# Performance work log

Hardware: AMD Instinct MI355X
Metric: run time of the kernel (lower is better)

## Reference

```python
import jax, jax.numpy as jnp
import numpy as np

VOCAB, D, HEADS, FF, LAYERS = 30522, 768, 12, 3072, 4
CHUNK, OVERLAP, EXT = 50, 7, 64
SAMPLE_N, TOPK, PAD = 8, 3, 0
MU = jnp.array([1.0, 0.9, 0.7, 0.5, 0.3, 0.1, -0.1, -0.3, -0.5, -0.7, -0.9], jnp.float32)
SIGMA = 0.1


def layernorm(x, g, b, eps=1e-12):
    m = x.mean(-1, keepdims=True)
    v = ((x - m) ** 2).mean(-1, keepdims=True)
    return (x - m) * jax.lax.rsqrt(v + eps) * g + b


def ck_context(x, conv_w, conv_b):
    # ConstantPad1d((0,2)) + Conv1d(k=3) + ReLU + L2-normalize; x: [..., L, D]
    L = x.shape[-2]
    pad = [(0, 0)] * (x.ndim - 2) + [(0, 2), (0, 0)]
    xp = jnp.pad(x, pad)
    y = conv_b + sum(jnp.einsum('...li,io->...lo', xp[..., k:k + L, :], conv_w[k]) for k in range(3))
    y = jax.nn.relu(y)
    return y / jnp.maximum(jnp.linalg.norm(y, axis=-1, keepdims=True), 1e-12)


def bert_layer(x, mask, Wq, bq, Wk, bk, Wv, bv, Wo, bo, g1, be1, W1, bf1, W2, bf2, g2, be2):
    N, L, _ = x.shape
    dh = D // HEADS
    split = lambda h: h.reshape(N, L, HEADS, dh)
    q, k, v = split(x @ Wq + bq), split(x @ Wk + bk), split(x @ Wv + bv)
    s = jnp.einsum('nqhd,nkhd->nhqk', q, k) / jnp.sqrt(jnp.asarray(dh, x.dtype))
    s = jnp.where(mask[:, None, None, :], s, -1e4)
    ctx = jnp.einsum('nhqk,nkhd->nqhd', jax.nn.softmax(s, -1), v).reshape(N, L, D)
    x = layernorm(x + ctx @ Wo + bo, g1, be1)
    h = jax.nn.gelu(x @ W1 + bf1, approximate=False)
    return layernorm(x + h @ W2 + bf2, g2, be2)


def setup_inputs():
    ks = jax.random.split(jax.random.key(0), 24)
    B, Lq, Ldoc = 32, 30, 4000
    f = lambda i, shape, s=0.02: jax.random.normal(ks[i], shape, jnp.float32) * s
    lens = jax.random.randint(ks[20], (B, 1), 2000, Ldoc, jnp.int32)
    doc_ids = jax.random.randint(ks[1], (B, Ldoc), 1, VOCAB, jnp.int32)
    doc_ids = doc_ids * (jnp.arange(Ldoc)[None, :] < lens)  # variable-length docs, 0 = padding
    return {
        'query_ids': jax.random.randint(ks[0], (B, Lq), 1, VOCAB, jnp.int32),
        'query_mask': jnp.ones((B, Lq), jnp.int32),
        'doc_ids': doc_ids,
        'word_emb': f(2, (VOCAB, D)),
        'pos_emb': f(3, (512, D)),
        'emb_ln_g': jnp.ones((D,), jnp.float32), 'emb_ln_b': jnp.zeros((D,), jnp.float32),
        'conv_w': f(4, (3, D, D)), 'conv_b': jnp.zeros((D,), jnp.float32),
        'kernel_alpha': jnp.ones((11,), jnp.float32),
        'binw_w': jax.random.uniform(ks[5], (1, 11), jnp.float32, -0.01, 0.01),
        'binw_b': jnp.zeros((1,), jnp.float32),
        'cls_w': f(6, (1, D)), 'cls_b': jnp.zeros((1,), jnp.float32),
        'topk_w': jnp.ones((1, TOPK), jnp.float32),
        'Wq': f(7, (LAYERS, D, D)), 'bq': jnp.zeros((LAYERS, D), jnp.float32),
        'Wk': f(8, (LAYERS, D, D)), 'bk': jnp.zeros((LAYERS, D), jnp.float32),
        'Wv': f(9, (LAYERS, D, D)), 'bv': jnp.zeros((LAYERS, D), jnp.float32),
        'Wo': f(10, (LAYERS, D, D)), 'bo': jnp.zeros((LAYERS, D), jnp.float32),
        'ln1_g': jnp.ones((LAYERS, D), jnp.float32), 'ln1_b': jnp.zeros((LAYERS, D), jnp.float32),
        'W1': f(11, (LAYERS, D, FF)), 'bf1': jnp.zeros((LAYERS, FF), jnp.float32),
        'W2': f(12, (LAYERS, FF, D)), 'bf2': jnp.zeros((LAYERS, D), jnp.float32),
        'ln2_g': jnp.ones((LAYERS, D), jnp.float32), 'ln2_b': jnp.zeros((LAYERS, D), jnp.float32),
    }


def reference(query_ids, query_mask, doc_ids, word_emb, pos_emb, emb_ln_g, emb_ln_b,
              conv_w, conv_b, kernel_alpha, binw_w, binw_b, cls_w, cls_b, topk_w,
              Wq, bq, Wk, bk, Wv, bv, Wo, bo, ln1_g, ln1_b, W1, bf1, W2, bf2, ln2_g, ln2_b):
    emb = lambda ids: layernorm(word_emb[ids] + pos_emb[:ids.shape[-1]], emb_ln_g, emb_ln_b)
    d_ids = doc_ids[:, 1:]
    B, Ld0 = d_ids.shape
    Lq = query_ids.shape[1]
    pad_r = EXT - (Ld0 % CHUNK - OVERLAP)  # Ld0 > overlap branch
    d_ids = jnp.pad(d_ids, ((0, 0), (OVERLAP, pad_r)))
    P = (d_ids.shape[1] - EXT) // CHUNK + 1
    win = np.arange(P)[:, None] * CHUNK + np.arange(EXT)[None, :]
    chunks = d_ids[:, win]                                   # [B,P,EXT] (unfold)
    valid = (chunks[..., OVERLAP:-OVERLAP] != PAD).any(-1)   # packed_indices, [B,P]
    chunk_mask = chunks != PAD
    # --- CK kernel-pooling sampler (embeddings detached) ---
    q_ctx = ck_context(jax.lax.stop_gradient(emb(query_ids)), conv_w, conv_b)  # [B,Lq,D]
    d_ctx = ck_context(jax.lax.stop_gradient(emb(chunks)), conv_w, conv_b)     # [B,P,EXT,D]
    cos = jnp.einsum('bqd,bped->bpqe', q_ctx, d_ctx)
    kact = jnp.exp(-(cos[..., None] - MU) ** 2 / (2 * SIGMA ** 2)) * chunk_mask[:, :, None, :, None]
    kres = jnp.log(jnp.maximum(kact.sum(3) * kernel_alpha, 1e-4)) * query_mask[:, None, :, None]
    samp = kres.sum(2) @ binw_w[0] + binw_b[0]               # [B,P]
    samp = jnp.where(valid, samp, 0.0)                       # zeros where not packed
    samp = jnp.where(samp == 0.0, -9000.0, samp)
    # --- top-k chunk routing into BERT (eval path, no cache) ---
    top_idx = jnp.argsort(-samp, axis=1)[:, :SAMPLE_N]       # [B,n]
    sel_ids = jnp.take_along_axis(chunks, top_idx[:, :, None], axis=1).reshape(B * SAMPLE_N, EXT)
    sel_valid = jnp.take_along_axis(valid, top_idx, axis=1)
    qi = jnp.broadcast_to(query_ids[:, None, :], (B, SAMPLE_N, Lq)).reshape(B * SAMPLE_N, Lq)
    qm = jnp.broadcast_to(query_mask[:, None, :], (B, SAMPLE_N, Lq)).reshape(B * SAMPLE_N, Lq)
    ids = jnp.concatenate([qi, sel_ids], 1)                  # [B*n, Lq+EXT]
    am = jnp.concatenate([qm != 0, sel_ids != PAD], 1)
    x = emb(ids)
    for i in range(LAYERS):
        x = bert_layer(x, am, Wq[i], bq[i], Wk[i], bk[i], Wv[i], bv[i], Wo[i], bo[i],
                       ln1_g[i], ln1_b[i], W1[i], bf1[i], W2[i], bf2[i], ln2_g[i], ln2_b[i])
    bscore = (x[:, 0] @ cls_w[0] + cls_b[0]).reshape(B, SAMPLE_N)
    bscore = jax.lax.stop_gradient(bscore)  # torch.set_grad_enabled(False) around BERT path
    bscore = jnp.where(sel_valid, bscore, 0.0)
    scores = jnp.zeros((B, P), bscore.dtype).at[jnp.arange(B)[:, None], top_idx].set(bscore)
    scores = jnp.where(scores == 0.0, -9000.0, scores)
    ssorted = -jnp.sort(-scores, axis=1)
    ssorted = jnp.where(ssorted <= -8900.0, 0.0, ssorted)
    return (ssorted[:, :TOPK] * topk_w[0]).sum(1)            # [B]
```

## Files before the change

### kernel.cpp

```cpp
#include <hip/hip_runtime.h>
#include <hip/hip_bf16.h>
#include <cstring>
#include <cmath>

#define NBAT 32
#define LQ 30
#define NP 80
#define NSEGC 2560
#define DD 768
#define KC 6912
#define LB 94
#define FF 3072

typedef unsigned short u16;
typedef __attribute__((__ext_vector_type__(4))) float f32x4;
typedef __attribute__((__ext_vector_type__(8))) short s16x8;
typedef __attribute__((__ext_vector_type__(8))) _Float16 f16x8;

__constant__ float MU_C[11] = {1.0f,0.9f,0.7f,0.5f,0.3f,0.1f,-0.1f,-0.3f,-0.5f,-0.7f,-0.9f};

__device__ __forceinline__ float wsum(float v) {
#pragma unroll
  for (int o = 32; o; o >>= 1) v += __shfl_xor(v, o);
  return v;
}
__device__ __forceinline__ u16 f2b(float f) {
  __hip_bfloat16 h = __float2bfloat16(f);
  u16 u; __builtin_memcpy(&u, &h, 2); return u;
}
__device__ __forceinline__ u16 h_bits(_Float16 h) { u16 u; __builtin_memcpy(&u, &h, 2); return u; }

__device__ __forceinline__ void gll16(const void* g, void* l) {
  __builtin_amdgcn_global_load_lds((const __attribute__((address_space(1))) unsigned*)g,
                                   (__attribute__((address_space(3))) unsigned*)l, 16, 0, 0);
}

template<int AMODE, int DT, int EPI>
__global__ __launch_bounds__(512) void gemm_mid(const u16* __restrict__ A, const u16* __restrict__ BT,
                                                void* __restrict__ Cv, const float* __restrict__ bias,
                                                int M, int N, int K)
{
  __shared__ __align__(16) u16 As[2][128*64];
  __shared__ __align__(16) u16 Bs[2][192*64];
  const int tid = threadIdx.x;
  const int lane = tid & 63;
  const int w = tid >> 6;

  const int NBY = N / 192;
  const int nb = gridDim.x;
  const int q8 = nb >> 3, r8 = nb & 7;
  const int xcd = blockIdx.x & 7, slot = blockIdx.x >> 3;
  const int base8 = (xcd < r8) ? xcd*(q8+1) : r8*(q8+1) + (xcd - r8)*q8;
  const int wk = base8 + slot;
  const long m0 = (long)(wk / NBY) * 128;
  const long n0 = (long)(wk % NBY) * 192;

  const int wr = (w >> 2) * 64;
  const int wc = (w & 3) * 48;

  const int lrow = lane >> 3;
  const int scg  = (lane & 7) ^ lrow;

  long aoff[2], boff[3];
#pragma unroll
  for (int it = 0; it < 2; ++it) {
    const long ga = m0 + it*64 + w*8 + lrow;
    if (AMODE == 0) aoff[it] = ga * (long)K;
    else            aoff[it] = ((ga >> 6) * 66 + (ga & 63)) * 2304L;
  }
#pragma unroll
  for (int it = 0; it < 3; ++it)
    boff[it] = (long)(n0 + it*64 + w*8 + lrow) * (long)K;

  f32x4 acc[4][3] = {};

  const int T = K >> 6;
#pragma unroll
  for (int it = 0; it < 2; ++it)
    gll16(A + aoff[it] + scg*8, &As[0][(it*64 + w*8) * 64]);
#pragma unroll
  for (int it = 0; it < 3; ++it)
    gll16(BT + boff[it] + scg*8, &Bs[0][(it*64 + w*8) * 64]);

  for (int t = 0; t < T; ++t) {
    const int cb = t & 1;
    if (t + 1 < T) {
      const int k1 = (t + 1) << 6;
#pragma unroll
      for (int it = 0; it < 2; ++it)
        gll16(A + aoff[it] + k1 + scg*8, &As[cb ^ 1][(it*64 + w*8) * 64]);
#pragma unroll
      for (int it = 0; it < 3; ++it)
        gll16(BT + boff[it] + k1 + scg*8, &Bs[cb ^ 1][(it*64 + w*8) * 64]);
      asm volatile("s_waitcnt vmcnt(5)" ::: "memory");
    } else {
      asm volatile("s_waitcnt vmcnt(0)" ::: "memory");
    }
    __builtin_amdgcn_s_barrier();
    __builtin_amdgcn_sched_barrier(0);
#pragma unroll
    for (int kk = 0; kk < 2; ++kk) {
      const int cc = kk*4 + (lane >> 4);
      const int sw = (cc ^ (lane & 7)) * 8;
      if constexpr (DT == 0) {
        s16x8 af[4], bg[3];
#pragma unroll
        for (int m = 0; m < 4; ++m)
          af[m] = *(const s16x8*)&As[cb][(wr + m*16 + (lane & 15))*64 + sw];
#pragma unroll
        for (int n = 0; n < 3; ++n)
          bg[n] = *(const s16x8*)&Bs[cb][(wc + n*16 + (lane & 15))*64 + sw];
#pragma unroll
        for (int m = 0; m < 4; ++m)
#pragma unroll
          for (int n = 0; n < 3; ++n)
            acc[m][n] = __builtin_amdgcn_mfma_f32_16x16x32_bf16(af[m], bg[n], acc[m][n], 0, 0, 0);
      } else {
        f16x8 af[4], bg[3];
#pragma unroll
        for (int m = 0; m < 4; ++m)
          af[m] = *(const f16x8*)&As[cb][(wr + m*16 + (lane & 15))*64 + sw];
#pragma unroll
        for (int n = 0; n < 3; ++n)
          bg[n] = *(const f16x8*)&Bs[cb][(wc + n*16 + (lane & 15))*64 + sw];
#pragma unroll
        for (int m = 0; m < 4; ++m)
#pragma unroll
          for (int n = 0; n < 3; ++n)
            acc[m][n] = __builtin_amdgcn_mfma_f32_16x16x32_f16(af[m], bg[n], acc[m][n], 0, 0, 0);
      }
    }
    __builtin_amdgcn_sched_barrier(0);
    __builtin_amdgcn_s_barrier();
  }
#pragma unroll
  for (int m = 0; m < 4; ++m) {
    const long r0 = m0 + wr + m*16 + (lane >> 4)*4;
#pragma unroll
    for (int n = 0; n < 3; ++n) {
      const long c = n0 + wc + n*16 + (lane & 15);
#pragma unroll
      for (int j = 0; j < 4; ++j) {
        const float val = acc[m][n][j];
        if constexpr (EPI == 0) {
          ((float*)Cv)[(r0 + j) * (long)N + c] = val;
        } else if constexpr (EPI == 1) {
          const float tg = val + bias[c];
          ((u16*)Cv)[(r0 + j) * (long)N + c] = f2b(0.5f * tg * (1.0f + erff(tg * 0.70710678118654752440f)));
        } else if constexpr (EPI == 2) {
          ((u16*)Cv)[(r0 + j) * (long)N + c] = f2b(val);
        } else {
          ((u16*)Cv)[(r0 + j) * (long)N + c] = f2b(val + bias[c]);
        }
      }
    }
  }
  (void)M;
}

__global__ __launch_bounds__(256) void k_transpose_tile(const float* __restrict__ src, u16* __restrict__ dst,
                                                        int K, int N)
{
  __shared__ float tile[64][65];
  const int kb = blockIdx.x * 64, nb = blockIdx.y * 64;
  const int tx = threadIdx.x & 63, ty = threadIdx.x >> 6;
#pragma unroll
  for (int r = ty; r < 64; r += 4)
    tile[r][tx] = src[(long)(kb + r) * N + nb + tx];
  __syncthreads();
#pragma unroll
  for (int r = ty; r < 64; r += 4)
    dst[(long)(nb + r) * K + kb + tx] = f2b(tile[tx][r]);
}

__global__ __launch_bounds__(256) void k_pack_w3t_tile(const float* __restrict__ conv_w, u16* __restrict__ w3t)
{
  __shared__ float tile[64][65];
  const int t = blockIdx.z;
  const int db = blockIdx.x * 64, ob = blockIdx.y * 64;
  const int tx = threadIdx.x & 63, ty = threadIdx.x >> 6;
#pragma unroll
  for (int r = ty; r < 64; r += 4)
    tile[r][tx] = conv_w[((long)t * 768 + db + r) * 768 + ob + tx];
  __syncthreads();
#pragma unroll
  for (int r = ty; r < 64; r += 4) {
    const float wv = tile[tx][r];
    const _Float16 hi = (_Float16)wv;
    const u16 uh = h_bits(hi);
    const u16 ul = h_bits((_Float16)(wv - (float)hi));
    u16* p = &w3t[(long)(ob + r) * KC + t * 2304 + (db + tx) * 3];
    p[0] = uh; p[1] = uh; p[2] = ul;
  }
}

__global__ void k_pack_qkvbias(const float* __restrict__ bq, const float* __restrict__ bk,
                               const float* __restrict__ bv, float* __restrict__ dst)
{
  const int idx = blockIdx.x*256 + threadIdx.x;
  if (idx >= 4*2304) return;
  const int L = idx / 2304, c = idx % 2304;
  const float* src = (c < 768) ? bq : (c < 1536 ? bk : bv);
  dst[idx] = src[L*768 + (c % 768)];
}

__global__ void k_build_chunks(const int* __restrict__ doc_ids, int* __restrict__ chunks, int* __restrict__ valid)
{
  const int bp = blockIdx.x;
  const int b = bp / NP, p = bp % NP;
  const int e = threadIdx.x;
  const int j = p*50 + e;
  int id = 0;
  const int di = j - 6;
  if (j >= 7 && di < 4000) id = doc_ids[b*4000 + di];
  chunks[bp*64 + e] = id;
  const unsigned long long bal = __ballot(e >= 7 && e < 57 && id != 0);
  if (e == 0) valid[bp] = (bal != 0ULL) ? 1 : 0;
}

__global__ __launch_bounds__(256) void k_emb_conv(const int* __restrict__ chunks,
    const int* __restrict__ query_ids, const float* __restrict__ word_emb,
    const float* __restrict__ pos_emb, const float* __restrict__ g,
    const float* __restrict__ bb, u16* __restrict__ A3, int seg0, int nT)
{
  const int Tl = blockIdx.x*4 + (threadIdx.x >> 6);
  if (Tl >= nT) return;
  const int lane = threadIdx.x & 63;
  const int seg = seg0 + Tl / 66, tok = Tl % 66;
  int id = -1;
  if (seg < NSEGC) { if (tok < 64) id = chunks[seg*64 + tok]; }
  else             { if (tok < LQ) id = query_ids[(seg - NSEGC)*LQ + tok]; }
  const long ob = (long)Tl * 2304;
  if (id < 0) {
#pragma unroll
    for (int j = 0; j < 12; ++j) {
      const int d = lane + 64*j;
      A3[ob + d*3 + 0] = 0; A3[ob + d*3 + 1] = 0; A3[ob + d*3 + 2] = 0;
    }
    return;
  }
  float v[12]; float s = 0.f;
#pragma unroll
  for (int j = 0; j < 12; ++j) {
    const int d = lane + 64*j;
    v[j] = word_emb[(long)id*DD + d] + pos_emb[(long)tok*DD + d];
    s += v[j];
  }
  s = wsum(s);
  const float mean = s * (1.f/768.f);
  float q = 0.f;
#pragma unroll
  for (int j = 0; j < 12; ++j) { const float t = v[j] - mean; q += t*t; }
  q = wsum(q);
  const float rstd = 1.f / sqrtf(q * (1.f/768.f) + 1e-12f);
#pragma unroll
  for (int j = 0; j < 12; ++j) {
    const int d = lane + 64*j;
    const float y = (v[j] - mean) * rstd * g[d] + bb[d];
    const _Float16 hi = (_Float16)y;
    const _Float16 lo = (_Float16)(y - (float)hi);
    const u16 uh = h_bits(hi);
    A3[ob + d*3 + 0] = uh;
    A3[ob + d*3 + 1] = h_bits(lo);
    A3[ob + d*3 + 2] = uh;
  }
}

__global__ __launch_bounds__(256) void k_conv_epi(float* __restrict__ Y, const float* __restrict__ cb)
{
  const int r = blockIdx.x*4 + (threadIdx.x >> 6);
  const int lane = threadIdx.x & 63;
  const long base = (long)r * DD;
  float v[12]; float ss = 0.f;
#pragma unroll
  for (int j = 0; j < 12; ++j) {
    const int d = lane + 64*j;
    float t = Y[base + d] + cb[d];
    t = fmaxf(t, 0.f);
    v[j] = t; ss += t*t;
  }
  ss = wsum(ss);
  const float sc = 1.f / fmaxf(sqrtf(ss), 1e-12f);
#pragma unroll
  for (int j = 0; j < 12; ++j) Y[base + lane + 64*j] = v[j]*sc;
}

__global__ __launch_bounds__(256) void k_cos_pool(const float* __restrict__ Ys,
    const float* __restrict__ qctx, const int* __restrict__ chunks, const int* __restrict__ valid,
    const int* __restrict__ query_mask, const float* __restrict__ alpha,
    const float* __restrict__ binw_w, const float* __restrict__ binw_b,
    float* __restrict__ samp, int seg0)
{
  __shared__ float Qs[15*768];
  __shared__ float cosm[30*64];
  __shared__ float maskf[64];
  __shared__ float qmw[32];
  __shared__ float red[4];
  const int bp = seg0 + blockIdx.x;
  const int b = bp / NP;
  const int tid = threadIdx.x, lane = tid & 63, w = tid >> 6;
  if (tid < 64) maskf[tid] = (chunks[bp*64 + tid] != 0) ? 1.f : 0.f;
  if (tid < LQ) qmw[tid] = (float)query_mask[b*LQ + tid];
  const long dbase = (long)blockIdx.x * 64 * DD;
  const long qrow0 = (long)b * 64;
  for (int pass = 0; pass < 2; ++pass) {
    const int q0 = pass * 15;
    for (int idx = tid; idx < 15*768; idx += 256)
      Qs[idx] = qctx[(qrow0 + q0 + idx/768)*DD + (idx % 768)];
    __syncthreads();
    for (int e = w; e < 64; e += 4) {
      float acc[15];
#pragma unroll
      for (int q = 0; q < 15; ++q) acc[q] = 0.f;
#pragma unroll
      for (int j = 0; j < 12; ++j) {
        const float dv = Ys[dbase + (long)e*DD + lane + 64*j];
#pragma unroll
        for (int q = 0; q < 15; ++q)
          acc[q] += dv * Qs[q*768 + lane + 64*j];
      }
#pragma unroll
      for (int q = 0; q < 15; ++q) {
        const float sv = wsum(acc[q]);
        if (lane == q) cosm[(q0 + q)*64 + e] = sv;
      }
    }
    __syncthreads();
  }
  float part = 0.f;
  for (int pr = tid; pr < 330; pr += 256) {
    const int q = pr / 11, mi = pr % 11;
    const float mu = MU_C[mi];
    float ks = 0.f;
    for (int e = 0; e < 64; ++e) {
      const float c = cosm[q*64 + e] - mu;
      ks += expf(-c*c*50.f) * maskf[e];
    }
    part += logf(fmaxf(ks * alpha[mi], 1e-4f)) * qmw[q] * binw_w[mi];
  }
  part = wsum(part);
  if (lane == 0) red[w] = part;
  __syncthreads();
  if (tid == 0) {
    const float s = red[0] + red[1] + red[2] + red[3] + binw_b[0];
    samp[bp] = (valid[bp] != 0 && s != 0.f) ? s : -9000.0f;
  }
}

__global__ void k_top8(const float* __restrict__ samp, const int* __restrict__ valid,
                       int* __restrict__ topidx, int* __restrict__ selv)
{
  const int b = blockIdx.x;
  const int l = threadIdx.x;
  float v1 = samp[b*NP + l];
  float v2 = (l < NP - 64) ? samp[b*NP + 64 + l] : -3e38f;
  for (int r = 0; r < 8; ++r) {
    float cv; int ci;
    if (v2 > v1) { cv = v2; ci = l + 64; } else { cv = v1; ci = l; }
#pragma unroll
    for (int o = 32; o; o >>= 1) {
      const float ov = __shfl_xor(cv, o);
      const int   oi = __shfl_xor(ci, o);
      if (ov > cv || (ov == cv && oi < ci)) { cv = ov; ci = oi; }
    }
    if (l == 0) { topidx[b*8 + r] = ci; selv[b*8 + r] = valid[b*NP + ci]; }
    if (ci == l)      v1 = -3e38f;
    if (ci == l + 64) v2 = -3e38f;
  }
}

__global__ __launch_bounds__(256) void k_bert_emb(const int* __restrict__ chunks,
    const int* __restrict__ query_ids, const int* __restrict__ query_mask,
    const int* __restrict__ topidx, const float* __restrict__ word_emb,
    const float* __restrict__ pos_emb, const float* __restrict__ g, const float* __restrict__ bb,
    float* __restrict__ xf, u16* __restrict__ xb, int* __restrict__ am, int n0)
{
  const int Tl = blockIdx.x*4 + (threadIdx.x >> 6);
  const int lane = threadIdx.x & 63;
  const int nl = Tl / LB, l = Tl % LB;
  const int n = n0 + nl;
  const int b = n >> 3, jj = n & 7;
  int id, amv;
  if (l < LQ) { id = query_ids[b*LQ + l]; amv = (query_mask[b*LQ + l] != 0) ? 1 : 0; }
  else { const int p = topidx[b*8 + jj]; id = chunks[(b*NP + p)*64 + (l - LQ)]; amv = (id != 0) ? 1 : 0; }
  if (lane == 0) am[n*LB + l] = amv;
  const long ob = (long)Tl * DD;
  float v[12]; float s = 0.f;
#pragma unroll
  for (int j = 0; j < 12; ++j) {
    const int d = lane + 64*j;
    v[j] = word_emb[(long)id*DD + d] + pos_emb[(long)l*DD + d];
    s += v[j];
  }
  s = wsum(s);
  const float mean = s * (1.f/768.f);
  float q = 0.f;
#pragma unroll
  for (int j = 0; j < 12; ++j) { const float t = v[j] - mean; q += t*t; }
  q = wsum(q);
  const float rstd = 1.f / sqrtf(q*(1.f/768.f) + 1e-12f);
#pragma unroll
  for (int j = 0; j < 12; ++j) {
    const int d = lane + 64*j;
    const float y = (v[j] - mean)*rstd*g[d] + bb[d];
    xf[ob + d] = y;
    xb[ob + d] = f2b(y);
  }
}

__global__ __launch_bounds__(384) void k_attn_mfma(const u16* __restrict__ qkvb,
    const int* __restrict__ am, u16* __restrict__ ctxb, int n0)
{
  __shared__ __align__(16) u16 Kb[96*72];
  __shared__ __align__(16) u16 Vt[64*104];
  __shared__ __align__(16) u16 Pl[6*16*104];
  __shared__ float maskb[96];
  const int nb = blockIdx.x;
  const int nl = nb / 12, h = nb % 12;
  const int tid = threadIdx.x, lane = tid & 63, w = tid >> 6;
  const int hoff = h * 64;
  const long rowbase = (long)nl * LB;

  for (int idx = tid; idx < 96*8; idx += 384) {
    const int l = idx >> 3, seg = idx & 7;
    s16x8 z = {};
    if (l < LB) z = *(const s16x8*)&qkvb[(rowbase + l)*2304 + 768 + hoff + seg*8];
    *(s16x8*)&Kb[l*72 + seg*8] = z;
  }
  for (int idx = tid; idx < 96*64; idx += 384) {
    const int j = idx >> 6, d = idx & 63;
    Vt[d*104 + j] = (j < LB) ? qkvb[(rowbase + j)*2304 + 1536 + hoff + d] : (u16)0;
  }
  if (tid < 96) maskb[tid] = (tid < LB && am[(n0 + nl)*LB + tid] != 0) ? 1.f : 0.f;
  __syncthreads();

  const int rt = w;
  s16x8 qf0, qf1;
  {
    int r = rt*16 + (lane & 15); if (r > LB-1) r = LB-1;
    const long qbase = (rowbase + r)*2304 + hoff + (lane >> 4)*8;
    qf0 = *(const s16x8*)&qkvb[qbase];
    qf1 = *(const s16x8*)&qkvb[qbase + 32];
  }
  f32x4 sa[6];
#pragma unroll
  for (int ct = 0; ct < 6; ++ct) {
    sa[ct] = f32x4{0.f,0.f,0.f,0.f};
    const int krow = ct*16 + (lane & 15);
    const s16x8 kf0 = *(const s16x8*)&Kb[krow*72 + (lane >> 4)*8];
    const s16x8 kf1 = *(const s16x8*)&Kb[krow*72 + 32 + (lane >> 4)*8];
    sa[ct] = __builtin_amdgcn_mfma_f32_16x16x32_bf16(qf0, kf0, sa[ct], 0, 0, 0);
    sa[ct] = __builtin_amdgcn_mfma_f32_16x16x32_bf16(qf1, kf1, sa[ct], 0, 0, 0);
  }
  float sv[6][4];
#pragma unroll
  for (int ct = 0; ct < 6; ++ct) {
    const int col = ct*16 + (lane & 15);
    const float mk = maskb[col];
#pragma unroll
    for (int j = 0; j < 4; ++j)
      sv[ct][j] = (mk != 0.f) ? sa[ct][j]*0.125f : -1.0e30f;
  }
  float mx[4], sm[4];
#pragma unroll
  for (int j = 0; j < 4; ++j) {
    float v = sv[0][j];
#pragma unroll
    for (int ct = 1; ct < 6; ++ct) v = fmaxf(v, sv[ct][j]);
#pragma unroll
    for (int o = 1; o < 16; o <<= 1) v = fmaxf(v, __shfl_xor(v, o));
    mx[j] = v;
  }
#pragma unroll
  for (int j = 0; j < 4; ++j) {
    float s = 0.f;
#pragma unroll
    for (int ct = 0; ct < 6; ++ct) { const float p = expf(sv[ct][j] - mx[j]); sv[ct][j] = p; s += p; }
#pragma unroll
    for (int o = 1; o < 16; o <<= 1) s += __shfl_xor(s, o);
    sm[j] = 1.f / s;
  }
  u16* Pw = &Pl[w*16*104];
#pragma unroll
  for (int ct = 0; ct < 6; ++ct)
#pragma unroll
    for (int j = 0; j < 4; ++j)
      Pw[((lane >> 4)*4 + j)*104 + ct*16 + (lane & 15)] = f2b(sv[ct][j]*sm[j]);
  asm volatile("s_waitcnt lgkmcnt(0)" ::: "memory");
  f32x4 oa[4];
#pragma unroll
  for (int nt = 0; nt < 4; ++nt) oa[nt] = f32x4{0.f,0.f,0.f,0.f};
#pragma unroll
  for (int ks = 0; ks < 3; ++ks) {
    const s16x8 pf = *(const s16x8*)&Pw[(lane & 15)*104 + ks*32 + (lane >> 4)*8];
#pragma unroll
    for (int nt = 0; nt < 4; ++nt) {
      const s16x8 vf = *(const s16x8*)&Vt[(nt*16 + (lane & 15))*104 + ks*32 + (lane >> 4)*8];
      oa[nt] = __builtin_amdgcn_mfma_f32_16x16x32_bf16(pf, vf, oa[nt], 0, 0, 0);
    }
  }
#pragma unroll
  for (int nt = 0; nt < 4; ++nt)
#pragma unroll
    for (int j = 0; j < 4; ++j) {
      const int r = rt*16 + (lane >> 4)*4 + j;
      if (r < LB)
        ctxb[(rowbase + r)*768 + hoff + nt*16 + (lane & 15)] = f2b(oa[nt][j]);
    }
}

__global__ __launch_bounds__(256) void k_ln(const float* __restrict__ resid,
    const float* __restrict__ gout, const float* __restrict__ bias,
    const float* __restrict__ g, const float* __restrict__ bb,
    float* __restrict__ of, u16* __restrict__ ob)
{
  const int r = blockIdx.x*4 + (threadIdx.x >> 6);
  const int lane = threadIdx.x & 63;
  const long base = (long)r * DD;
  float v[12]; float s = 0.f;
#pragma unroll
  for (int j = 0; j < 12; ++j) {
    const int d = lane + 64*j;
    v[j] = resid[base + d] + gout[base + d] + bias[d];
    s += v[j];
  }
  s = wsum(s);
  const float mean = s * (1.f/768.f);
  float q = 0.f;
#pragma unroll
  for (int j = 0; j < 12; ++j) { const float t = v[j] - mean; q += t*t; }
  q = wsum(q);
  const float rstd = 1.f / sqrtf(q*(1.f/768.f) + 1e-12f);
#pragma unroll
  for (int j = 0; j < 12; ++j) {
    const int d = lane + 64*j;
    const float y = (v[j] - mean)*rstd*g[d] + bb[d];
    of[base + d] = y;
    ob[base + d] = f2b(y);
  }
}

__global__ void k_cls(const float* __restrict__ xf, const float* __restrict__ cls_w,
                      const float* __restrict__ cls_b, float* __restrict__ bscore, int n0)
{
  const int nl = blockIdx.x*4 + (threadIdx.x >> 6);
  const int lane = threadIdx.x & 63;
  const long base = (long)nl * LB * DD;
  float s = 0.f;
#pragma unroll
  for (int j = 0; j < 12; ++j) { const int d = lane + 64*j; s += xf[base + d] * cls_w[d]; }
  s = wsum(s);
  if (lane == 0) bscore[n0 + nl] = s + cls_b[0];
}

__global__ void k_final(const float* __restrict__ bscore, const int* __restrict__ selv,
                        const float* __restrict__ topk_w, float* __restrict__ out)
{
  const int b = threadIdx.x;
  if (b >= NBAT) return;
  float t0 = -3e38f, t1 = -3e38f, t2 = -3e38f;
  for (int j = 0; j < 8; ++j) {
    const float bs = bscore[b*8 + j];
    const float v = (selv[b*8 + j] != 0 && bs != 0.0f) ? bs : -9000.0f;
    if (v > t0)      { t2 = t1; t1 = t0; t0 = v; }
    else if (v > t1) { t2 = t1; t1 = v; }
    else if (v > t2) { t2 = v; }
  }
  t0 = (t0 <= -8900.0f) ? 0.0f : t0;
  t1 = (t1 <= -8900.0f) ? 0.0f : t1;
  t2 = (t2 <= -8900.0f) ? 0.0f : t2;
  out[b] = t0*topk_w[0] + t1*topk_w[1] + t2*topk_w[2];
}

extern "C" void kernel_launch(void* const* d_in, const int* in_sizes, int n_in,
                              void* d_out, int out_size, void* d_ws, size_t ws_size,
                              hipStream_t stream)
{
  const int*   query_ids  = (const int*)d_in[0];
  const int*   query_mask = (const int*)d_in[1];
  const int*   doc_ids    = (const int*)d_in[2];
  const float* word_emb   = (const float*)d_in[3];
  const float* pos_emb    = (const float*)d_in[4];
  const float* emb_ln_g   = (const float*)d_in[5];
  const float* emb_ln_b   = (const float*)d_in[6];
  const float* conv_w     = (const float*)d_in[7];
  const float* conv_b     = (const float*)d_in[8];
  const float* kernel_alpha = (const float*)d_in[9];
  const float* binw_w     = (const float*)d_in[10];
  const float* binw_b     = (const float*)d_in[11];
  const float* cls_w      = (const float*)d_in[12];
  const float* cls_b      = (const float*)d_in[13];
  const float* topk_w     = (const float*)d_in[14];
  const float* Wq  = (const float*)d_in[15];
  const float* bq  = (const float*)d_in[16];
  const float* Wk  = (const float*)d_in[17];
  const float* bk  = (const float*)d_in[18];
  const float* Wv  = (const float*)d_in[19];
  const float* bv  = (const float*)d_in[20];
  const float* Wo  = (const float*)d_in[21];
  const float* bo  = (const float*)d_in[22];
  const float* ln1_g = (const float*)d_in[23];
  const float* ln1_b = (const float*)d_in[24];
  const float* W1  = (const float*)d_in[25];
  const float* bf1 = (const float*)d_in[26];
  const float* W2  = (const float*)d_in[27];
  const float* bf2 = (const float*)d_in[28];
  const float* ln2_g = (const float*)d_in[29];
  const float* ln2_b = (const float*)d_in[30];
  (void)in_sizes; (void)n_in; (void)out_size;

  char* ws = (char*)d_ws;
  size_t o = 0;
  auto take = [&](size_t bytes) { char* p = ws + o; o += bytes; return p; };
  int*   chunks = (int*)take(655360);
  int*   valid  = (int*)take(10240);
  float* samp   = (float*)take(10240);
  int*   topidx = (int*)take(1024);
  int*   selv   = (int*)take(1024);
  int*   am     = (int*)take(96256);
  float* bscore = (float*)take(1024);
  float* qctx   = (float*)take(6291456);
  float* qkvbias= (float*)take(36864);
  u16* w3t   = (u16*)take(10616832UL);
  u16* wqkvT = (u16*)take(14155776UL);
  u16* woT   = (u16*)take(4718592UL);
  u16* w1T   = (u16*)take(18874368UL);
  u16* w2T   = (u16*)take(18874368UL);
  const size_t persist = o;

  int BSL_ = 64;
  if (ws_size >= persist + (size_t)(256*LB) * 21504UL)      BSL_ = 256;
  else if (ws_size >= persist + (size_t)(128*LB) * 21504UL) BSL_ = 128;
  const int NSL2_ = 256 / BSL_;
  const long M2 = (long)BSL_ * LB;

  int CSL_ = 256;
  if (ws_size >= persist + 512UL * 500736UL) CSL_ = 512;
  const int NSL1_ = NSEGC / CSL_;
  const int MSL1_ = CSL_ * 64;

  char* U = ws + persist;
  u16*   A3s = (u16*)U;
  float* Ys  = (float*)(U + (size_t)CSL_ * 304128UL);
  u16*   qkvb   = (u16*)U;
  float* attn_o = (float*)U;
  float* xf  = (float*)(U + (size_t)M2*4608UL);
  float* x1f = (float*)(U + (size_t)M2*7680UL);
  u16*   xb  = (u16*)(U + (size_t)M2*10752UL);
  u16*   x1b = (u16*)(U + (size_t)M2*12288UL);
  u16*   ctxb= (u16*)(U + (size_t)M2*13824UL);
  u16*   hb  = (u16*)(U + (size_t)M2*15360UL);

  k_pack_w3t_tile<<<dim3(12, 12, 3), 256, 0, stream>>>(conv_w, w3t);
  k_pack_qkvbias<<<36, 256, 0, stream>>>(bq, bk, bv, qkvbias);
  for (int L = 0; L < 4; ++L) {
    k_transpose_tile<<<dim3(12,12), 256, 0, stream>>>(Wq + (size_t)L*768*768, wqkvT + (size_t)L*2304*768,            768, 768);
    k_transpose_tile<<<dim3(12,12), 256, 0, stream>>>(Wk + (size_t)L*768*768, wqkvT + (size_t)L*2304*768 + 768*768,  768, 768);
    k_transpose_tile<<<dim3(12,12), 256, 0, stream>>>(Wv + (size_t)L*768*768, wqkvT + (size_t)L*2304*768 + 1536*768, 768, 768);
    k_transpose_tile<<<dim3(12,12), 256, 0, stream>>>(Wo + (size_t)L*768*768, woT + (size_t)L*768*768, 768, 768);
    k_transpose_tile<<<dim3(12,48), 256, 0, stream>>>(W1 + (size_t)L*768*3072, w1T + (size_t)L*3072*768, 768, 3072);
    k_transpose_tile<<<dim3(48,12), 256, 0, stream>>>(W2 + (size_t)L*3072*768, w2T + (size_t)L*768*3072, 3072, 768);
  }

  k_build_chunks<<<NSEGC, 64, 0, stream>>>(doc_ids, chunks, valid);
  k_emb_conv<<<(NBAT*66)/4, 256, 0, stream>>>(chunks, query_ids, word_emb, pos_emb, emb_ln_g, emb_ln_b,
                                              A3s, NSEGC, NBAT*66);
  gemm_mid<1,1,0><<<(NBAT*64/128)*(DD/192), 512, 0, stream>>>(A3s, w3t, qctx, nullptr, NBAT*64, DD, KC);
  k_conv_epi<<<(NBAT*64)/4, 256, 0, stream>>>(qctx, conv_b);
  for (int s = 0; s < NSL1_; ++s) {
    const int seg0 = s * CSL_;
    k_emb_conv<<<(CSL_*66+3)/4, 256, 0, stream>>>(chunks, query_ids, word_emb, pos_emb, emb_ln_g, emb_ln_b,
                                                  A3s, seg0, CSL_*66);
    gemm_mid<1,1,0><<<(MSL1_/128)*(DD/192), 512, 0, stream>>>(A3s, w3t, Ys, nullptr, MSL1_, DD, KC);
    k_conv_epi<<<MSL1_/4, 256, 0, stream>>>(Ys, conv_b);
    k_cos_pool<<<CSL_, 256, 0, stream>>>(Ys, qctx, chunks, valid, query_mask, kernel_alpha,
                                         binw_w, binw_b, samp, seg0);
  }
  k_top8<<<NBAT, 64, 0, stream>>>(samp, valid, topidx, selv);

  for (int t = 0; t < NSL2_; ++t) {
    const int n0 = t * BSL_;
    k_bert_emb<<<(int)(M2/4), 256, 0, stream>>>(chunks, query_ids, query_mask, topidx, word_emb, pos_emb,
                                                emb_ln_g, emb_ln_b, xf, xb, am, n0);
    for (int L = 0; L < 4; ++L) {
      gemm_mid<0,0,3><<<(int)((M2/128)*(2304/192)), 512, 0, stream>>>(xb, wqkvT + (size_t)L*2304*768, qkvb, qkvbias + L*2304, (int)M2, 2304, 768);
      k_attn_mfma<<<BSL_*12, 384, 0, stream>>>(qkvb, am, ctxb, n0);
      gemm_mid<0,0,0><<<(int)((M2/128)*(768/192)), 512, 0, stream>>>(ctxb, woT + (size_t)L*768*768, attn_o, nullptr, (int)M2, 768, 768);
      k_ln<<<(int)(M2/4), 256, 0, stream>>>(xf, attn_o, bo + L*768, ln1_g + L*768, ln1_b + L*768, x1f, x1b);
      gemm_mid<0,0,1><<<(int)((M2/128)*(3072/192)), 512, 0, stream>>>(x1b, w1T + (size_t)L*3072*768, hb, bf1 + L*3072, (int)M2, 3072, 768);
      gemm_mid<0,0,0><<<(int)((M2/128)*(768/192)), 512, 0, stream>>>(hb, w2T + (size_t)L*768*3072, attn_o, nullptr, (int)M2, 768, 3072);
      k_ln<<<(int)(M2/4), 256, 0, stream>>>(x1f, attn_o, bf2 + L*768, ln2_g + L*768, ln2_b + L*768, xf, xb);
    }
    k_cls<<<BSL_/4, 256, 0, stream>>>(xf, cls_w, cls_b, bscore, n0);
  }
  k_final<<<1, 64, 0, stream>>>(bscore, selv, topk_w, (float*)d_out);
}
```

Baseline: 5.635 ms.

## Use 4-wave GEMM tiles, fuse conv epilogue into cos-pool, batch weight transposes

The shared GEMM kernel moves from 8 waves of 64x48 subtiles to 4 waves of 64x96 subtiles. Each wave now reuses its A fragments across twice as many MFMAs, at the cost of more accumulator registers and fewer waves to hide latency. The conv bias, ReLU and L2 normalization are folded into k_cos_pool, which removes a separate pass that read and wrote the whole conv output. The 24 weight-transpose launches are merged into three batched launches to cut launch overhead.

```diff
diff --git a/kernel.cpp b/kernel.cpp
--- a/kernel.cpp
+++ b/kernel.cpp
@@ -36,7 +36,7 @@
 }
 
 template<int AMODE, int DT, int EPI>
-__global__ __launch_bounds__(512) void gemm_mid(const u16* __restrict__ A, const u16* __restrict__ BT,
+__global__ __launch_bounds__(256) void gemm_mid(const u16* __restrict__ A, const u16* __restrict__ BT,
                                                 void* __restrict__ Cv, const float* __restrict__ bias,
                                                 int M, int N, int K)
 {
@@ -55,44 +55,44 @@
   const long m0 = (long)(wk / NBY) * 128;
   const long n0 = (long)(wk % NBY) * 192;
 
-  const int wr = (w >> 2) * 64;
-  const int wc = (w & 3) * 48;
+  const int wr = (w >> 1) * 64;
+  const int wc = (w & 1) * 96;
 
   const int lrow = lane >> 3;
   const int scg  = (lane & 7) ^ lrow;
 
-  long aoff[2], boff[3];
-#pragma unroll
-  for (int it = 0; it < 2; ++it) {
-    const long ga = m0 + it*64 + w*8 + lrow;
+  long aoff[4], boff[6];
+#pragma unroll
+  for (int it = 0; it < 4; ++it) {
+    const long ga = m0 + w*32 + it*8 + lrow;
     if (AMODE == 0) aoff[it] = ga * (long)K;
     else            aoff[it] = ((ga >> 6) * 66 + (ga & 63)) * 2304L;
   }
 #pragma unroll
-  for (int it = 0; it < 3; ++it)
-    boff[it] = (long)(n0 + it*64 + w*8 + lrow) * (long)K;
-
-  f32x4 acc[4][3] = {};
+  for (int it = 0; it < 6; ++it)
+    boff[it] = (long)(n0 + w*48 + it*8 + lrow) * (long)K;
+
+  f32x4 acc[4][6] = {};
 
   const int T = K >> 6;
 #pragma unroll
-  for (int it = 0; it < 2; ++it)
-    gll16(A + aoff[it] + scg*8, &As[0][(it*64 + w*8) * 64]);
-#pragma unroll
-  for (int it = 0; it < 3; ++it)
-    gll16(BT + boff[it] + scg*8, &Bs[0][(it*64 + w*8) * 64]);
+  for (int it = 0; it < 4; ++it)
+    gll16(A + aoff[it] + scg*8, &As[0][(w*32 + it*8) * 64]);
+#pragma unroll
+  for (int it = 0; it < 6; ++it)
+    gll16(BT + boff[it] + scg*8, &Bs[0][(w*48 + it*8) * 64]);
 
   for (int t = 0; t < T; ++t) {
     const int cb = t & 1;
     if (t + 1 < T) {
       const int k1 = (t + 1) << 6;
 #pragma unroll
-      for (int it = 0; it < 2; ++it)
-        gll16(A + aoff[it] + k1 + scg*8, &As[cb ^ 1][(it*64 + w*8) * 64]);
-#pragma unroll
-      for (int it = 0; it < 3; ++it)
-        gll16(BT + boff[it] + k1 + scg*8, &Bs[cb ^ 1][(it*64 + w*8) * 64]);
-      asm volatile("s_waitcnt vmcnt(5)" ::: "memory");
+      for (int it = 0; it < 4; ++it)
+        gll16(A + aoff[it] + k1 + scg*8, &As[cb ^ 1][(w*32 + it*8) * 64]);
+#pragma unroll
+      for (int it = 0; it < 6; ++it)
+        gll16(BT + boff[it] + k1 + scg*8, &Bs[cb ^ 1][(w*48 + it*8) * 64]);
+      asm volatile("s_waitcnt vmcnt(10)" ::: "memory");
     } else {
       asm volatile("s_waitcnt vmcnt(0)" ::: "memory");
     }
@@ -103,30 +103,30 @@
       const int cc = kk*4 + (lane >> 4);
       const int sw = (cc ^ (lane & 7)) * 8;
       if constexpr (DT == 0) {
-        s16x8 af[4], bg[3];
+        s16x8 af[4], bg[6];
 #pragma unroll
         for (int m = 0; m < 4; ++m)
           af[m] = *(const s16x8*)&As[cb][(wr + m*16 + (lane & 15))*64 + sw];
 #pragma unroll
-        for (int n = 0; n < 3; ++n)
+        for (int n = 0; n < 6; ++n)
           bg[n] = *(const s16x8*)&Bs[cb][(wc + n*16 + (lane & 15))*64 + sw];
 #pragma unroll
         for (int m = 0; m < 4; ++m)
 #pragma unroll
-          for (int n = 0; n < 3; ++n)
+          for (int n = 0; n < 6; ++n)
             acc[m][n] = __builtin_amdgcn_mfma_f32_16x16x32_bf16(af[m], bg[n], acc[m][n], 0, 0, 0);
       } else {
-        f16x8 af[4], bg[3];
+        f16x8 af[4], bg[6];
 #pragma unroll
         for (int m = 0; m < 4; ++m)
           af[m] = *(const f16x8*)&As[cb][(wr + m*16 + (lane & 15))*64 + sw];
 #pragma unroll
-        for (int n = 0; n < 3; ++n)
+        for (int n = 0; n < 6; ++n)
           bg[n] = *(const f16x8*)&Bs[cb][(wc + n*16 + (lane & 15))*64 + sw];
 #pragma unroll
         for (int m = 0; m < 4; ++m)
 #pragma unroll
-          for (int n = 0; n < 3; ++n)
+          for (int n = 0; n < 6; ++n)
             acc[m][n] = __builtin_amdgcn_mfma_f32_16x16x32_f16(af[m], bg[n], acc[m][n], 0, 0, 0);
       }
     }
@@ -137,7 +137,7 @@
   for (int m = 0; m < 4; ++m) {
     const long r0 = m0 + wr + m*16 + (lane >> 4)*4;
 #pragma unroll
-    for (int n = 0; n < 3; ++n) {
+    for (int n = 0; n < 6; ++n) {
       const long c = n0 + wc + n*16 + (lane & 15);
 #pragma unroll
       for (int j = 0; j < 4; ++j) {
@@ -158,19 +158,57 @@
   (void)M;
 }
 
-__global__ __launch_bounds__(256) void k_transpose_tile(const float* __restrict__ src, u16* __restrict__ dst,
-                                                        int K, int N)
+__global__ __launch_bounds__(256) void k_transpose_qkvo(const float* __restrict__ Wq, const float* __restrict__ Wk,
+                                                        const float* __restrict__ Wv, const float* __restrict__ Wo,
+                                                        u16* __restrict__ wqkvT, u16* __restrict__ woT)
 {
   __shared__ float tile[64][65];
+  const int z = blockIdx.z, L = z >> 2, t = z & 3;
+  const float* src = ((t == 0) ? Wq : (t == 1) ? Wk : (t == 2) ? Wv : Wo) + (size_t)L*768*768;
+  u16* dst = (t < 3) ? (wqkvT + (size_t)L*2304*768 + (size_t)t*768*768) : (woT + (size_t)L*768*768);
   const int kb = blockIdx.x * 64, nb = blockIdx.y * 64;
   const int tx = threadIdx.x & 63, ty = threadIdx.x >> 6;
 #pragma unroll
   for (int r = ty; r < 64; r += 4)
-    tile[r][tx] = src[(long)(kb + r) * N + nb + tx];
+    tile[r][tx] = src[(long)(kb + r) * 768 + nb + tx];
   __syncthreads();
 #pragma unroll
   for (int r = ty; r < 64; r += 4)
-    dst[(long)(nb + r) * K + kb + tx] = f2b(tile[tx][r]);
+    dst[(long)(nb + r) * 768 + kb + tx] = f2b(tile[tx][r]);
+}
+
+__global__ __launch_bounds__(256) void k_transpose_w1(const float* __restrict__ W1, u16* __restrict__ w1T)
+{
+  __shared__ float tile[64][65];
+  const int L = blockIdx.z;
+  const float* src = W1 + (size_t)L*768*3072;
+  u16* dst = w1T + (size_t)L*3072*768;
+  const int kb = blockIdx.x * 64, nb = blockIdx.y * 64;
+  const int tx = threadIdx.x & 63, ty = threadIdx.x >> 6;
+#pragma unroll
+  for (int r = ty; r < 64; r += 4)
+    tile[r][tx] = src[(long)(kb + r) * 3072 + nb + tx];
+  __syncthreads();
+#pragma unroll
+  for (int r = ty; r < 64; r += 4)
+    dst[(long)(nb + r) * 768 + kb + tx] = f2b(tile[tx][r]);
+}
+
+__global__ __launch_bounds__(256) void k_transpose_w2(const float* __restrict__ W2, u16* __restrict__ w2T)
+{
+  __shared__ float tile[64][65];
+  const int L = blockIdx.z;
+  const float* src = W2 + (size_t)L*3072*768;
+  u16* dst = w2T + (size_t)L*768*3072;
+  const int kb = blockIdx.x * 64, nb = blockIdx.y * 64;
+  const int tx = threadIdx.x & 63, ty = threadIdx.x >> 6;
+#pragma unroll
+  for (int r = ty; r < 64; r += 4)
+    tile[r][tx] = src[(long)(kb + r) * 768 + nb + tx];
+  __syncthreads();
+#pragma unroll
+  for (int r = ty; r < 64; r += 4)
+    dst[(long)(nb + r) * 3072 + kb + tx] = f2b(tile[tx][r]);
 }
 
 __global__ __launch_bounds__(256) void k_pack_w3t_tile(const float* __restrict__ conv_w, u16* __restrict__ w3t)
@@ -285,14 +323,17 @@
   for (int j = 0; j < 12; ++j) Y[base + lane + 64*j] = v[j]*sc;
 }
 
-__global__ __launch_bounds__(256) void k_cos_pool(const float* __restrict__ Ys,
-    const float* __restrict__ qctx, const int* __restrict__ chunks, const int* __restrict__ valid,
+__global__ __launch_bounds__(256) void k_cos_pool(const float* __restrict__ Yraw,
+    const float* __restrict__ cb, const float* __restrict__ qctx,
+    const int* __restrict__ chunks, const int* __restrict__ valid,
     const int* __restrict__ query_mask, const float* __restrict__ alpha,
     const float* __restrict__ binw_w, const float* __restrict__ binw_b,
     float* __restrict__ samp, int seg0)
 {
   __shared__ float Qs[15*768];
   __shared__ float cosm[30*64];
+  __shared__ float cbs[768];
+  __shared__ float normv[64];
   __shared__ float maskf[64];
   __shared__ float qmw[32];
   __shared__ float red[4];
@@ -301,6 +342,7 @@
   const int tid = threadIdx.x, lane = tid & 63, w = tid >> 6;
   if (tid < 64) maskf[tid] = (chunks[bp*64 + tid] != 0) ? 1.f : 0.f;
   if (tid < LQ) qmw[tid] = (float)query_mask[b*LQ + tid];
+  for (int idx = tid; idx < 768; idx += 256) cbs[idx] = cb[idx];
   const long dbase = (long)blockIdx.x * 64 * DD;
   const long qrow0 = (long)b * 64;
   for (int pass = 0; pass < 2; ++pass) {
@@ -312,17 +354,28 @@
       float acc[15];
 #pragma unroll
       for (int q = 0; q < 15; ++q) acc[q] = 0.f;
+      float nrm = 0.f;
 #pragma unroll
       for (int j = 0; j < 12; ++j) {
-        const float dv = Ys[dbase + (long)e*DD + lane + 64*j];
+        const int d = lane + 64*j;
+        const float dv = fmaxf(Yraw[dbase + (long)e*DD + d] + cbs[d], 0.f);
+        nrm += dv*dv;
 #pragma unroll
         for (int q = 0; q < 15; ++q)
-          acc[q] += dv * Qs[q*768 + lane + 64*j];
+          acc[q] += dv * Qs[q*768 + d];
+      }
+      float rn;
+      if (pass == 0) {
+        nrm = wsum(nrm);
+        rn = 1.f / fmaxf(sqrtf(nrm), 1e-12f);
+        if (lane == 32) normv[e] = rn;
+      } else {
+        rn = normv[e];
       }
 #pragma unroll
       for (int q = 0; q < 15; ++q) {
         const float sv = wsum(acc[q]);
-        if (lane == q) cosm[(q0 + q)*64 + e] = sv;
+        if (lane == q) cosm[(q0 + q)*64 + e] = sv * rn;
       }
     }
     __syncthreads();
@@ -653,27 +706,21 @@
 
   k_pack_w3t_tile<<<dim3(12, 12, 3), 256, 0, stream>>>(conv_w, w3t);
   k_pack_qkvbias<<<36, 256, 0, stream>>>(bq, bk, bv, qkvbias);
-  for (int L = 0; L < 4; ++L) {
-    k_transpose_tile<<<dim3(12,12), 256, 0, stream>>>(Wq + (size_t)L*768*768, wqkvT + (size_t)L*2304*768,            768, 768);
-    k_transpose_tile<<<dim3(12,12), 256, 0, stream>>>(Wk + (size_t)L*768*768, wqkvT + (size_t)L*2304*768 + 768*768,  768, 768);
-    k_transpose_tile<<<dim3(12,12), 256, 0, stream>>>(Wv + (size_t)L*768*768, wqkvT + (size_t)L*2304*768 + 1536*768, 768, 768);
-    k_transpose_tile<<<dim3(12,12), 256, 0, stream>>>(Wo + (size_t)L*768*768, woT + (size_t)L*768*768, 768, 768);
-    k_transpose_tile<<<dim3(12,48), 256, 0, stream>>>(W1 + (size_t)L*768*3072, w1T + (size_t)L*3072*768, 768, 3072);
-    k_transpose_tile<<<dim3(48,12), 256, 0, stream>>>(W2 + (size_t)L*3072*768, w2T + (size_t)L*768*3072, 3072, 768);
-  }
+  k_transpose_qkvo<<<dim3(12,12,16), 256, 0, stream>>>(Wq, Wk, Wv, Wo, wqkvT, woT);
+  k_transpose_w1<<<dim3(12,48,4), 256, 0, stream>>>(W1, w1T);
+  k_transpose_w2<<<dim3(48,12,4), 256, 0, stream>>>(W2, w2T);
 
   k_build_chunks<<<NSEGC, 64, 0, stream>>>(doc_ids, chunks, valid);
   k_emb_conv<<<(NBAT*66)/4, 256, 0, stream>>>(chunks, query_ids, word_emb, pos_emb, emb_ln_g, emb_ln_b,
                                               A3s, NSEGC, NBAT*66);
-  gemm_mid<1,1,0><<<(NBAT*64/128)*(DD/192), 512, 0, stream>>>(A3s, w3t, qctx, nullptr, NBAT*64, DD, KC);
+  gemm_mid<1,1,0><<<(NBAT*64/128)*(DD/192), 256, 0, stream>>>(A3s, w3t, qctx, nullptr, NBAT*64, DD, KC);
   k_conv_epi<<<(NBAT*64)/4, 256, 0, stream>>>(qctx, conv_b);
   for (int s = 0; s < NSL1_; ++s) {
     const int seg0 = s * CSL_;
     k_emb_conv<<<(CSL_*66+3)/4, 256, 0, stream>>>(chunks, query_ids, word_emb, pos_emb, emb_ln_g, emb_ln_b,
                                                   A3s, seg0, CSL_*66);
-    gemm_mid<1,1,0><<<(MSL1_/128)*(DD/192), 512, 0, stream>>>(A3s, w3t, Ys, nullptr, MSL1_, DD, KC);
-    k_conv_epi<<<MSL1_/4, 256, 0, stream>>>(Ys, conv_b);
-    k_cos_pool<<<CSL_, 256, 0, stream>>>(Ys, qctx, chunks, valid, query_mask, kernel_alpha,
+    gemm_mid<1,1,0><<<(MSL1_/128)*(DD/192), 256, 0, stream>>>(A3s, w3t, Ys, nullptr, MSL1_, DD, KC);
+    k_cos_pool<<<CSL_, 256, 0, stream>>>(Ys, conv_b, qctx, chunks, valid, query_mask, kernel_alpha,
                                          binw_w, binw_b, samp, seg0);
   }
   k_top8<<<NBAT, 64, 0, stream>>>(samp, valid, topidx, selv);
@@ -683,12 +730,12 @@
     k_bert_emb<<<(int)(M2/4), 256, 0, stream>>>(chunks, query_ids, query_mask, topidx, word_emb, pos_emb,
                                                 emb_ln_g, emb_ln_b, xf, xb, am, n0);
     for (int L = 0; L < 4; ++L) {
-      gemm_mid<0,0,3><<<(int)((M2/128)*(2304/192)), 512, 0, stream>>>(xb, wqkvT + (size_t)L*2304*768, qkvb, qkvbias + L*2304, (int)M2, 2304, 768);
+      gemm_mid<0,0,3><<<(int)((M2/128)*(2304/192)), 256, 0, stream>>>(xb, wqkvT + (size_t)L*2304*768, qkvb, qkvbias + L*2304, (int)M2, 2304, 768);
       k_attn_mfma<<<BSL_*12, 384, 0, stream>>>(qkvb, am, ctxb, n0);
-      gemm_mid<0,0,0><<<(int)((M2/128)*(768/192)), 512, 0, stream>>>(ctxb, woT + (size_t)L*768*768, attn_o, nullptr, (int)M2, 768, 768);
+      gemm_mid<0,0,0><<<(int)((M2/128)*(768/192)), 256, 0, stream>>>(ctxb, woT + (size_t)L*768*768, attn_o, nullptr, (int)M2, 768, 768);
       k_ln<<<(int)(M2/4), 256, 0, stream>>>(xf, attn_o, bo + L*768, ln1_g + L*768, ln1_b + L*768, x1f, x1b);
-      gemm_mid<0,0,1><<<(int)((M2/128)*(3072/192)), 512, 0, stream>>>(x1b, w1T + (size_t)L*3072*768, hb, bf1 + L*3072, (int)M2, 3072, 768);
-      gemm_mid<0,0,0><<<(int)((M2/128)*(768/192)), 512, 0, stream>>>(hb, w2T + (size_t)L*768*3072, attn_o, nullptr, (int)M2, 768, 3072);
+      gemm_mid<0,0,1><<<(int)((M2/128)*(3072/192)), 256, 0, stream>>>(x1b, w1T + (size_t)L*3072*768, hb, bf1 + L*3072, (int)M2, 3072, 768);
+      gemm_mid<0,0,0><<<(int)((M2/128)*(768/192)), 256, 0, stream>>>(hb, w2T + (size_t)L*768*3072, attn_o, nullptr, (int)M2, 768, 3072);
       k_ln<<<(int)(M2/4), 256, 0, stream>>>(x1f, attn_o, bf2 + L*768, ln2_g + L*768, ln2_b + L*768, xf, xb);
     }
     k_cls<<<BSL_/4, 256, 0, stream>>>(xf, cls_w, cls_b, bscore, n0);
```

New measurement: 5.684 ms. Within noise of the previous version (+0.9%).
